# Kernel tuning notes

Hardware: AMD Instinct MI355X
Metric: run time of the kernel (lower is better)

## Reference

```python
import jax, jax.numpy as jnp
import numpy as np

N, E, G = 200000, 600000, 1024
NF_IN, EF_IN, H = 32, 16, 512
BN_EPS = 1e-5


def _bn(x, gamma, beta):
    # eval-mode BatchNorm1d with running_mean=0, running_var=1
    return x * (gamma / jnp.sqrt(1.0 + BN_EPS)) + beta


def setup_inputs() -> dict:
    key = jax.random.key(0)
    ks = jax.random.split(key, 32)
    s = 0.05
    inp = {
        'nf': jax.random.normal(ks[0], (N, NF_IN), jnp.float32),
        'ef': jax.random.normal(ks[1], (E, EF_IN), jnp.float32),
        'gf': jax.random.normal(ks[2], (G, H), jnp.float32),
        'device_params': jax.random.uniform(ks[3], (N,), jnp.float32),
        'node_y': jax.random.randint(ks[4], (N,), 0, 9),
        'batch_idx': jnp.sort(jax.random.randint(ks[5], (N,), 0, G)),
        'edge_index': jax.random.randint(ks[6], (2, E), 0, N),
        'nf_w1': jax.random.normal(ks[7], (NF_IN + 9, H), jnp.float32) * s,
        'nf_b1': jax.random.normal(ks[8], (H,), jnp.float32) * s,
        'nf_g1': jax.random.uniform(ks[9], (H,), jnp.float32, 0.5, 1.5),
        'nf_be1': jax.random.normal(ks[10], (H,), jnp.float32) * s,
        'nf_w2': jax.random.normal(ks[11], (H, H), jnp.float32) * s,
        'nf_b2': jax.random.normal(ks[12], (H,), jnp.float32) * s,
        'ef_w1': jax.random.normal(ks[13], (EF_IN, H), jnp.float32) * s,
        'ef_b1': jax.random.normal(ks[14], (H,), jnp.float32) * s,
        'ef_g1': jax.random.uniform(ks[15], (H,), jnp.float32, 0.5, 1.5),
        'ef_be1': jax.random.normal(ks[16], (H,), jnp.float32) * s,
        'ef_w2': jax.random.normal(ks[17], (H, H), jnp.float32) * s,
        'ef_b2': jax.random.normal(ks[18], (H,), jnp.float32) * s,
        'ow1': jax.random.normal(ks[19], (H, H), jnp.float32) * s,
        'ob1': jax.random.normal(ks[20], (H,), jnp.float32) * s,
        'og1': jax.random.uniform(ks[21], (H,), jnp.float32, 0.5, 1.5),
        'obe1': jax.random.normal(ks[22], (H,), jnp.float32) * s,
        'ow2': jax.random.normal(ks[23], (H, H), jnp.float32) * s,
        'ob2': jax.random.normal(ks[24], (H,), jnp.float32) * s,
        'og2': jax.random.uniform(ks[25], (H,), jnp.float32, 0.5, 1.5),
        'obe2': jax.random.normal(ks[26], (H,), jnp.float32) * s,
        'ow3': jax.random.normal(ks[27], (H, 2), jnp.float32) * s,
        'ob3': jax.random.normal(ks[28], (2,), jnp.float32) * s,
    }
    return inp


def reference(nf, ef, gf, device_params, node_y, batch_idx, edge_index,
              nf_w1, nf_b1, nf_g1, nf_be1, nf_w2, nf_b2,
              ef_w1, ef_b1, ef_g1, ef_be1, ef_w2, ef_b2,
              ow1, ob1, og1, obe1, ow2, ob2, og2, obe2, ow3, ob3):
    num_graphs = gf.shape[0]
    gelu = lambda x: jax.nn.gelu(x, approximate=False)  # torch nn.GELU default

    # DeviceParam_MLP: augment node features with scaled one-hot of node class
    nf_aug = jnp.concatenate(
        [nf, jax.nn.one_hot(node_y, 9, dtype=nf.dtype) * device_params[:, None]],
        axis=-1)  # [N, nf_in+9]
    h_n = gelu(_bn(nf_aug @ nf_w1 + nf_b1, nf_g1, nf_be1)) @ nf_w2 + nf_b2  # [N,H]
    h_e = gelu(_bn(ef @ ef_w1 + ef_b1, ef_g1, ef_be1)) @ ef_w2 + ef_b2      # [E,H]

    # two scatter_add pools into graph features
    gh = gf
    gh = gh + jax.ops.segment_sum(h_n, batch_idx, num_segments=num_graphs)
    edge_graph = batch_idx[edge_index[0]]  # graph id of each edge's source node
    gh = gh + jax.ops.segment_sum(h_e, edge_graph, num_segments=num_graphs)

    # output MLP (layer_num=3): two hidden blocks + final Linear -> 2
    x = gelu(_bn(gh @ ow1 + ob1, og1, obe1))
    x = gelu(_bn(x @ ow2 + ob2, og2, obe2))
    return x @ ow3 + ob3  # [G, 2]
```

## Files before the change

kernel.cpp:

```cpp
#include <hip/hip_runtime.h>
#include <hip/hip_bf16.h>
#include <cmath>

#define NN 200000
#define NE 600000
#define NG 1024
#define HH 512
#define ES 896

typedef short short8 __attribute__((ext_vector_type(8)));
typedef short short4v __attribute__((ext_vector_type(4)));
typedef float f32x4 __attribute__((ext_vector_type(4)));
typedef float f32x2 __attribute__((ext_vector_type(2)));
typedef float f32x16 __attribute__((ext_vector_type(16)));

__device__ __forceinline__ unsigned short f2bf(float f){
  unsigned u = __float_as_uint(f);
  u += 0x7fffu + ((u >> 16) & 1u);
  return (unsigned short)(u >> 16);
}
__device__ __forceinline__ float bf2f(unsigned short h){
  return __uint_as_float(((unsigned)h) << 16);
}

__device__ __forceinline__ short8 cvt8pk(float4 a, float4 b){
  union { short8 s; __hip_bfloat162 h[4]; } u;
  u.h[0] = __float22bfloat162_rn(make_float2(a.x, a.y));
  u.h[1] = __float22bfloat162_rn(make_float2(a.z, a.w));
  u.h[2] = __float22bfloat162_rn(make_float2(b.x, b.y));
  u.h[3] = __float22bfloat162_rn(make_float2(b.z, b.w));
  return u.s;
}

__device__ __forceinline__ float gelu_f(float x){
  float p = __builtin_fmaf(x*x, -0.10294325f, -2.3022085f);
  float e = __builtin_amdgcn_exp2f(x * p);
  return x * __builtin_amdgcn_rcpf(1.0f + e);
}

#define PKFMA3(d,a,b,c) asm("v_pk_fma_f32 %0, %1, %2, %3" : "=v"(d) : "v"(a), "v"(b), "v"(c))
#define PKFMA_IP(p,s,k) asm("v_pk_fma_f32 %0, %0, %1, %2" : "+v"(p) : "v"(s), "v"(k))
#define PKADD_IP(d,a)   asm("v_pk_add_f32 %0, %0, %1"     : "+v"(d) : "v"(a))

#define G2(y_) { \
  f32x2 s_; PKFMA3(s_, y_, y_, n1); \
  f32x2 p_; PKFMA3(p_, s_, K6, K5); \
  PKFMA_IP(p_, s_, K4); PKFMA_IP(p_, s_, K3); \
  PKFMA_IP(p_, s_, K2); PKFMA_IP(p_, s_, K1); \
  PKFMA_IP(p_, s_, K0); \
  PKADD_IP(aX, y_); PKADD_IP(aP, p_); }

#define COEFS \
  const f32x2 K0 = {c0,c0}, K1 = {c1,c1}, K2 = {c2,c2}, K3 = {c3,c3}; \
  const f32x2 K4 = {c4,c4}, K5 = {c5,c5}, K6 = {c6,c6}; \
  const f32x2 n1 = {-1.f,-1.f};

#define ISQ 0.56568542494924f
#define FXH 0.88388347648318f

__global__ __launch_bounds__(256) void kpre(
    const float* __restrict__ nfw1, const float* __restrict__ nfb1,
    const float* __restrict__ nfg1, const float* __restrict__ nfbe1,
    const float* __restrict__ efw1, const float* __restrict__ efb1,
    const float* __restrict__ efg1, const float* __restrict__ efbe1,
    const float* __restrict__ w2n, const float* __restrict__ w2e,
    const float* __restrict__ ow1, const float* __restrict__ ow2,
    unsigned short* __restrict__ w1n48T, unsigned short* __restrict__ w1eT16,
    float* __restrict__ b1n_s, float* __restrict__ b1e_s,
    const int* __restrict__ bidx, int* __restrict__ nstart,
    int* __restrict__ cnt,
    const float* __restrict__ nf, const float* __restrict__ dp,
    const int* __restrict__ ny,
    unsigned short* __restrict__ nf48,
    unsigned short* __restrict__ Bh1, unsigned short* __restrict__ Bl1,
    unsigned short* __restrict__ Bh2, unsigned short* __restrict__ Bl2,
    unsigned short* __restrict__ Bh3, unsigned short* __restrict__ Bl3){
  const float rs = 0.99999500003750f;
  int b = blockIdx.x, t = threadIdx.x;
  if (b < 2){
    int c = b*256 + t;
    float sc = efg1[c]*rs*ISQ;
#pragma unroll
    for (int k=0;k<16;++k) w1eT16[c*16+k] = f2bf(efw1[k*HH+c]*sc);
    b1e_s[c] = (efb1[c]*efg1[c]*rs + efbe1[c])*ISQ;
  } else if (b < 4){
    int c = (b-2)*256 + t;
    float sc = nfg1[c]*rs*ISQ;
#pragma unroll
    for (int k=0;k<48;++k)
      w1n48T[c*48+k] = (k < 41) ? f2bf(nfw1[k*HH+c]*sc) : (unsigned short)0;
    b1n_s[c] = (nfb1[c]*nfg1[c]*rs + nfbe1[c])*ISQ;
  } else if (b < 786){
    int i = (b-4)*256 + t;
    if (i < NN){
      int g0 = bidx[i];
      int g1 = (i+1 < NN) ? bidx[i+1] : NG;
      for (int g = g0+1; g <= g1; ++g) nstart[g] = i+1;
      if (i == 0) for (int g = 0; g <= g0; ++g) nstart[g] = 0;
    }
  } else if (b == 786){
    cnt[t] = 0; cnt[t+256] = 0; cnt[t+512] = 0; cnt[t+768] = 0;
  } else if (b < 1569){
    int r = (b-787)*256 + t;
    if (r < NN){
      const float4* ap = (const float4*)(nf + (size_t)r*32);
      unsigned short v[48];
      union { short8 s; unsigned short u[8]; } cv;
#pragma unroll
      for (int p2=0; p2<4; ++p2){
        cv.s = cvt8pk(ap[2*p2], ap[2*p2+1]);
#pragma unroll
        for (int j=0;j<8;++j) v[p2*8+j] = cv.u[j];
      }
      unsigned short db = f2bf(dp[r]);
      int cls = ny[r];
#pragma unroll
      for (int j=0;j<9;++j) v[32+j] = (cls==j) ? db : (unsigned short)0;
#pragma unroll
      for (int j=41;j<48;++j) v[j] = 0;
      unsigned short* op = nf48 + (size_t)r*48;
#pragma unroll
      for (int p2=0; p2<6; ++p2) *(short8*)(op + p2*8) = *(short8*)&v[p2*8];
    }
  } else {
    __shared__ float lds[64][65];
    int tb = b - 1569;
    int which, KK; unsigned short *Th, *Tl;
    if (tb < 128){ which = 1; KK = 1024; Th = Bh1; Tl = Bl1; }
    else if (tb < 192){ which = 2; KK = 512; Th = Bh2; Tl = Bl2; tb -= 128; }
    else { which = 3; KK = 512; Th = Bh3; Tl = Bl3; tb -= 192; }
    const int kt = tb >> 3, ct = tb & 7;
    const int k0 = kt*64, c0 = ct*64;
    const int tr = t >> 4, tc = (t & 15)*4;
#pragma unroll
    for (int i=0;i<4;++i){
      int row = tr + i*16;
      int gk = k0 + row;
      const float* src;
      if (which == 1) src = (gk < 512) ? (w2n + (size_t)gk*HH) : (w2e + (size_t)(gk-512)*HH);
      else if (which == 2) src = ow1 + (size_t)gk*HH;
      else src = ow2 + (size_t)gk*HH;
      float4 v = *(const float4*)(src + c0 + tc);
      lds[row][tc+0] = v.x; lds[row][tc+1] = v.y;
      lds[row][tc+2] = v.z; lds[row][tc+3] = v.w;
    }
    __syncthreads();
#pragma unroll
    for (int i=0;i<4;++i){
      int c = tr + i*16;
      short4v h4, l4;
#pragma unroll
      for (int j=0;j<4;++j){
        float vv = lds[tc+j][c];
        unsigned short h = f2bf(vv);
        h4[j] = (short)h;
        l4[j] = (short)f2bf(vv - bf2f(h));
      }
      size_t o = (size_t)(c0 + c)*KK + k0 + tc;
      *(short4v*)(Th + o) = h4;
      *(short4v*)(Tl + o) = l4;
    }
  }
}

__global__ __launch_bounds__(1024) void kscatter(const int* __restrict__ eidx,
    const int* __restrict__ bidx, const float* __restrict__ ef,
    int* __restrict__ eg, int* __restrict__ cnt, unsigned short* __restrict__ efs){
  __shared__ int h[NG];
  __shared__ int base[NG];
  const int b = blockIdx.x, t = threadIdx.x;
  h[t] = 0;
  __syncthreads();
  const int per = NE / 64;
  const int lo = b*per, hi = lo + per;
  for (int e = lo + t; e < hi; e += 1024){
    int g = bidx[eidx[e]];
    eg[e] = g;
    atomicAdd(&h[g], 1);
  }
  __syncthreads();
  int c = h[t];
  if (c > 0) base[t] = atomicAdd(&cnt[t], c);
  h[t] = 0;
  __syncthreads();
  for (int e = lo + t; e < hi; e += 1024){
    int g = eg[e];
    int p = base[g] + atomicAdd(&h[g], 1);
    if (p < ES){
      const float4* ap = (const float4*)(ef + (size_t)e*16);
      float4 a0 = ap[0], a1 = ap[1], a2 = ap[2], a3 = ap[3];
      unsigned short* op = efs + ((size_t)g*ES + p)*16;
      *(short8*)op       = cvt8pk(a0, a1);
      *(short8*)(op + 8) = cvt8pk(a2, a3);
    }
  }
}

__global__ __launch_bounds__(512) void kmain2(
    const unsigned short* __restrict__ efs, const int* __restrict__ cnt,
    const unsigned short* __restrict__ w1eT16, const float* __restrict__ b1e_s,
    const unsigned short* __restrict__ nf48, const int* __restrict__ nstart,
    const unsigned short* __restrict__ w1n48T, const float* __restrict__ b1n_s,
    float c0, float c1, float c2, float c3, float c4, float c5, float c6,
    unsigned short* __restrict__ Sh, unsigned short* __restrict__ Sl){
  const int t = threadIdx.x;
  const int lane = t & 63, wid = t >> 6;
  const int hi = lane >> 5, ln31 = lane & 31;
  COEFS;
  f32x2 aX = {0.f,0.f}, aP = {0.f,0.f};
  if (blockIdx.x < 2048){
    const int g = blockIdx.x >> 1;
    const int col = ((blockIdx.x & 1) << 8) + (wid << 5) + ln31;
    short8 bfr = *(const short8*)(w1eT16 + col*16 + (hi<<3));
    const float bv = b1e_s[col];
    f32x16 bias16;
#pragma unroll
    for (int i=0;i<16;++i) bias16[i] = bv;
    const int s1 = min(cnt[g], ES);
    const unsigned short* ep = efs + (size_t)g*(ES*16) + ln31*16 + (hi<<3);
    const int nfull = s1 >> 5;
    int rb = 0;
    for (int ch=0; ch<nfull; ++ch, rb += 32){
      short8 af = *(const short8*)(ep + rb*16);
      f32x16 acc = __builtin_amdgcn_mfma_f32_32x32x16_bf16(af, bfr, bias16, 0, 0, 0);
#pragma unroll
      for (int i=0;i<8;++i){
        f32x2 y = {acc[2*i], acc[2*i+1]};
        G2(y);
      }
    }
    if (rb < s1){
      int row = min(rb + ln31, s1-1);
      short8 af = *(const short8*)(efs + (size_t)g*(ES*16) + row*16 + (hi<<3));
      f32x16 acc = __builtin_amdgcn_mfma_f32_32x32x16_bf16(af, bfr, bias16, 0, 0, 0);
      const int vr = s1 - rb;
#pragma unroll
      for (int i=0;i<8;++i){
        int r0 = ((2*i)&3) + (((2*i)>>2)<<3) + (hi<<2);
        f32x2 y = { (r0 < vr) ? acc[2*i] : 0.f,
                    (r0+1 < vr) ? acc[2*i+1] : 0.f };
        G2(y);
      }
    }
    float ssum = __builtin_fmaf(FXH, aX[0]+aX[1], aP[0]+aP[1]);
    ssum += __shfl_xor(ssum, 32);
    if (lane < 32){
      size_t o = (size_t)g*1024 + 512 + col;
      unsigned short h = f2bf(ssum);
      Sh[o] = h; Sl[o] = f2bf(ssum - bf2f(h));
    }
  } else {
    const int b2 = blockIdx.x - 2048;
    const int g = b2 >> 1;
    const int col = ((b2 & 1) << 8) + (wid << 5) + ln31;
    const unsigned short* bp = w1n48T + col*48 + (hi<<3);
    short8 b0 = *(const short8*)(bp);
    short8 b1 = *(const short8*)(bp + 16);
    short8 b2f = *(const short8*)(bp + 32);
    const float bv = b1n_s[col];
    f32x16 bias16;
#pragma unroll
    for (int i=0;i<16;++i) bias16[i] = bv;
    const int s0r = nstart[g], s1 = nstart[g+1];
    const int nch = (s1 - s0r + 31) >> 5;
    for (int ch=0; ch<nch; ++ch){
      const int rb = s0r + ch*32;
      int ar = min(rb + ln31, s1-1);
      const unsigned short* apn = nf48 + (size_t)ar*48 + (hi<<3);
      short8 a0 = *(const short8*)(apn);
      short8 a1 = *(const short8*)(apn + 16);
      short8 a2 = *(const short8*)(apn + 32);
      f32x16 acc = __builtin_amdgcn_mfma_f32_32x32x16_bf16(a0, b0, bias16, 0, 0, 0);
      acc = __builtin_amdgcn_mfma_f32_32x32x16_bf16(a1, b1, acc, 0, 0, 0);
      acc = __builtin_amdgcn_mfma_f32_32x32x16_bf16(a2, b2f, acc, 0, 0, 0);
      const int vr = s1 - rb;
      if (vr >= 32){
#pragma unroll
        for (int i=0;i<8;++i){
          f32x2 y = {acc[2*i], acc[2*i+1]};
          G2(y);
        }
      } else {
#pragma unroll
        for (int i=0;i<8;++i){
          int r0 = ((2*i)&3) + (((2*i)>>2)<<3) + (hi<<2);
          f32x2 y = { (r0 < vr) ? acc[2*i] : 0.f,
                      (r0+1 < vr) ? acc[2*i+1] : 0.f };
          G2(y);
        }
      }
    }
    float ssum = __builtin_fmaf(FXH, aX[0]+aX[1], aP[0]+aP[1]);
    ssum += __shfl_xor(ssum, 32);
    if (lane < 32){
      size_t o = (size_t)g*1024 + col;
      unsigned short h = f2bf(ssum);
      Sh[o] = h; Sl[o] = f2bf(ssum - bf2f(h));
    }
  }
}

__global__ __launch_bounds__(256) void kg(
    const unsigned short* __restrict__ Ah, const unsigned short* __restrict__ Al,
    int K, int nkc,
    const unsigned short* __restrict__ Bh, const unsigned short* __restrict__ Bl,
    const float* __restrict__ gf, const int* __restrict__ nstart, const int* __restrict__ cnt,
    const float* __restrict__ b2n, const float* __restrict__ b2e,
    const float* __restrict__ bias, const float* __restrict__ gam, const float* __restrict__ bet,
    unsigned short* __restrict__ Oh, unsigned short* __restrict__ Ol,
    float* __restrict__ outf){
  const int t = threadIdx.x, lane = t & 63, w = t >> 6;
  const int q = lane >> 4, m = lane & 15;
  const int flat = blockIdx.y*32 + blockIdx.x;
  const int swz = (flat & 7)*64 + (flat >> 3);
  const int c0 = (swz & 31)*16, r0 = (swz >> 5)*64 + w*16;
  f32x4 acc = {0.f,0.f,0.f,0.f};
  const unsigned short* ahp = Ah + (size_t)(r0 + m)*K + (q<<3);
  const unsigned short* alp = Al + (size_t)(r0 + m)*K + (q<<3);
  const unsigned short* bhp = Bh + (size_t)(c0 + m)*K + (q<<3);
  const unsigned short* blp = Bl + (size_t)(c0 + m)*K + (q<<3);
#pragma unroll 2
  for (int kc = 0; kc < nkc; ++kc){
    const int ko = kc*32;
    short8 ah = *(const short8*)(ahp + ko);
    short8 al = *(const short8*)(alp + ko);
    short8 bh = *(const short8*)(bhp + ko);
    short8 bl = *(const short8*)(blp + ko);
    acc = __builtin_amdgcn_mfma_f32_16x16x32_bf16(ah, bh, acc, 0, 0, 0);
    acc = __builtin_amdgcn_mfma_f32_16x16x32_bf16(ah, bl, acc, 0, 0, 0);
    acc = __builtin_amdgcn_mfma_f32_16x16x32_bf16(al, bh, acc, 0, 0, 0);
  }
  const float rs = 0.99999500003750f;
  const int c = c0 + m;
  if (gf){
    const float bnv = b2n[c], bev = b2e[c];
#pragma unroll
    for (int i=0;i<4;++i){
      int r = r0 + q*4 + i;
      float cn = (float)(nstart[r+1] - nstart[r]);
      float ce = (float)min(cnt[r], ES);
      float v = acc[i] + gf[(size_t)r*HH + c] + cn*bnv + ce*bev;
      unsigned short h = f2bf(v);
      Oh[(size_t)r*HH + c] = h;
      Ol[(size_t)r*HH + c] = f2bf(v - bf2f(h));
    }
  } else {
    const float sc = gam[c]*rs, bi = bias[c], be = bet[c];
#pragma unroll
    for (int i=0;i<4;++i){
      int r = r0 + q*4 + i;
      float v = gelu_f((acc[i] + bi)*sc + be);
      if (outf) outf[(size_t)r*HH + c] = v;
      else {
        unsigned short h = f2bf(v);
        Oh[(size_t)r*HH + c] = h;
        Ol[(size_t)r*HH + c] = f2bf(v - bf2f(h));
      }
    }
  }
}

__global__ __launch_bounds__(256) void kfinal(const float* __restrict__ x2, const float* __restrict__ w3,
    const float* __restrict__ b3, float* __restrict__ out){
  const int lane = threadIdx.x & 63, wv = threadIdx.x >> 6;
  const int r = blockIdx.x*4 + wv;
  float a0 = 0.f, a1 = 0.f;
#pragma unroll
  for (int tt=0; tt<8; ++tt){
    int k = lane + tt*64;
    float x = x2[(size_t)r*HH + k];
    a0 = __builtin_fmaf(x, w3[2*k], a0);
    a1 = __builtin_fmaf(x, w3[2*k+1], a1);
  }
#pragma unroll
  for (int d=1; d<64; d<<=1){ a0 += __shfl_xor(a0, d); a1 += __shfl_xor(a1, d); }
  if (lane == 0){ out[r*2] = a0 + b3[0]; out[r*2+1] = a1 + b3[1]; }
}

extern "C" void kernel_launch(void* const* d_in, const int* in_sizes, int n_in,
                              void* d_out, int out_size, void* d_ws, size_t ws_size,
                              hipStream_t stream) {
  const float* nf    = (const float*)d_in[0];
  const float* ef    = (const float*)d_in[1];
  const float* gf    = (const float*)d_in[2];
  const float* dp    = (const float*)d_in[3];
  const int*   ny    = (const int*)d_in[4];
  const int*   bidx  = (const int*)d_in[5];
  const int*   eidx  = (const int*)d_in[6];
  const float* nfw1  = (const float*)d_in[7];
  const float* nfb1  = (const float*)d_in[8];
  const float* nfg1  = (const float*)d_in[9];
  const float* nfbe1 = (const float*)d_in[10];
  const float* w2n   = (const float*)d_in[11];
  const float* b2n   = (const float*)d_in[12];
  const float* efw1  = (const float*)d_in[13];
  const float* efb1  = (const float*)d_in[14];
  const float* efg1  = (const float*)d_in[15];
  const float* efbe1 = (const float*)d_in[16];
  const float* w2e   = (const float*)d_in[17];
  const float* b2e   = (const float*)d_in[18];
  const float* ow1   = (const float*)d_in[19];
  const float* ob1   = (const float*)d_in[20];
  const float* og1   = (const float*)d_in[21];
  const float* obe1  = (const float*)d_in[22];
  const float* ow2   = (const float*)d_in[23];
  const float* ob2   = (const float*)d_in[24];
  const float* og2   = (const float*)d_in[25];
  const float* obe2  = (const float*)d_in[26];
  const float* ow3   = (const float*)d_in[27];
  const float* ob3   = (const float*)d_in[28];

  static float MC[7];
  static bool inited = false;
  if (!inited){
    const double PI = 3.14159265358979323846;
    double th[7], fj[7];
    for (int j=0;j<7;++j){
      th[j] = PI*((double)j + 0.5)/7.0;
      double u = 3.125*(cos(th[j]) + 1.0);
      double v = sqrt(u);
      fj[j] = 0.5*v*erf(v*0.70710678118654752);
    }
    double c[7];
    for (int k=0;k<7;++k){
      double sm = 0.0;
      for (int j=0;j<7;++j) sm += fj[j]*cos((double)k*th[j]);
      c[k] = 2.0*sm/7.0;
    }
    c[0] *= 0.5;
    const double T[7][7] = {
      { 1, 0,  0,  0,   0,  0,  0},
      { 0, 1,  0,  0,   0,  0,  0},
      {-1, 0,  2,  0,   0,  0,  0},
      { 0,-3,  0,  4,   0,  0,  0},
      { 1, 0, -8,  0,   8,  0,  0},
      { 0, 5,  0,-20,   0, 16,  0},
      {-1, 0, 18,  0, -48,  0, 32}};
    double m[7] = {0,0,0,0,0,0,0};
    for (int k=0;k<7;++k)
      for (int i=0;i<7;++i) m[i] += c[k]*T[k][i];
    double p1 = m[0]-m[1]+m[2]-m[3]+m[4]-m[5]+m[6];
    m[0] -= p1;
    for (int i=0;i<7;++i) MC[i] = (float)m[i];
    inited = true;
  }

  unsigned char* p = (unsigned char*)d_ws;
  unsigned short* Sh = (unsigned short*)p;   p += (size_t)NG*1024*2;
  unsigned short* Sl = (unsigned short*)p;   p += (size_t)NG*1024*2;
  unsigned short* efs = (unsigned short*)p;  p += (size_t)NG*ES*16*2;
  unsigned short* nf48 = (unsigned short*)p; p += (size_t)NN*48*2;
  unsigned short* Bh1 = (unsigned short*)p;  p += (size_t)HH*1024*2;
  unsigned short* Bl1 = (unsigned short*)p;  p += (size_t)HH*1024*2;
  unsigned short* Bh2 = (unsigned short*)p;  p += (size_t)HH*512*2;
  unsigned short* Bl2 = (unsigned short*)p;  p += (size_t)HH*512*2;
  unsigned short* Bh3 = (unsigned short*)p;  p += (size_t)HH*512*2;
  unsigned short* Bl3 = (unsigned short*)p;  p += (size_t)HH*512*2;
  unsigned short* w1n48T = (unsigned short*)p; p += 512*48*2;
  unsigned short* w1eT16 = (unsigned short*)p; p += 512*16*2;
  float* b1n_s  = (float*)p;                 p += 512*4;
  float* b1e_s  = (float*)p;                 p += 512*4;
  int* nstart   = (int*)p;                   p += 1032*4;
  int* cnt      = (int*)p;                   p += NG*4;
  int* eg = (int*)Sh;
  unsigned short* ghh = (unsigned short*)nf48;
  unsigned short* ghl = ghh + (size_t)NG*HH;
  unsigned short* xgh = ghl + (size_t)NG*HH;
  unsigned short* xgl = xgh + (size_t)NG*HH;
  float* x2f = (float*)(xgl + (size_t)NG*HH);

  kpre<<<1825, 256, 0, stream>>>(nfw1, nfb1, nfg1, nfbe1, efw1, efb1, efg1, efbe1,
                                 w2n, w2e, ow1, ow2,
                                 w1n48T, w1eT16, b1n_s, b1e_s, bidx, nstart, cnt,
                                 nf, dp, ny, nf48,
                                 Bh1, Bl1, Bh2, Bl2, Bh3, Bl3);
  kscatter<<<64, 1024, 0, stream>>>(eidx, bidx, ef, eg, cnt, efs);
  kmain2<<<4096, 512, 0, stream>>>(efs, cnt, w1eT16, b1e_s,
                                   nf48, nstart, w1n48T, b1n_s,
                                   MC[0], MC[1], MC[2], MC[3], MC[4], MC[5], MC[6],
                                   Sh, Sl);
  kg<<<dim3(32,16), 256, 0, stream>>>(Sh, Sl, 1024, 32, Bh1, Bl1,
                                      gf, nstart, cnt, b2n, b2e,
                                      nullptr, nullptr, nullptr, ghh, ghl, nullptr);
  kg<<<dim3(32,16), 256, 0, stream>>>(ghh, ghl, 512, 16, Bh2, Bl2,
                                      nullptr, nullptr, nullptr, nullptr, nullptr,
                                      ob1, og1, obe1, xgh, xgl, nullptr);
  kg<<<dim3(32,16), 256, 0, stream>>>(xgh, xgl, 512, 16, Bh3, Bl3,
                                      nullptr, nullptr, nullptr, nullptr, nullptr,
                                      ob2, og2, obe2, nullptr, nullptr, x2f);
  kfinal<<<NG/4, 256, 0, stream>>>(x2f, ow3, ob3, (float*)d_out);
}
```

Measured before the change: 372.9 us.

## Fuse final linear layer into last GEMM epilogue and prefetch edge tiles

Removes the separate final kernel. The last GEMM epilogue now multiplies each GELU output by the two output weights, reduces across the 16 columns with shuffles, and atomically adds into the output, which kpre pre-fills with the bias. It also software-prefetches the next 32-row edge tile in the edge MLP loop and pads the edge buffer so the overrun read stays in bounds. This saves a kernel launch and the fp32 intermediate round trip, at the cost of float atomics that make the summation order nondeterministic.

```diff
diff --git a/kernel.cpp b/kernel.cpp
--- a/kernel.cpp
+++ b/kernel.cpp
@@ -65,6 +65,7 @@
     const float* __restrict__ efg1, const float* __restrict__ efbe1,
     const float* __restrict__ w2n, const float* __restrict__ w2e,
     const float* __restrict__ ow1, const float* __restrict__ ow2,
+    const float* __restrict__ ob3, float* __restrict__ outd,
     unsigned short* __restrict__ w1n48T, unsigned short* __restrict__ w1eT16,
     float* __restrict__ b1n_s, float* __restrict__ b1e_s,
     const int* __restrict__ bidx, int* __restrict__ nstart,
@@ -100,6 +101,8 @@
     }
   } else if (b == 786){
     cnt[t] = 0; cnt[t+256] = 0; cnt[t+512] = 0; cnt[t+768] = 0;
+    float bb0 = ob3[0], bb1 = ob3[1];
+    for (int i = t; i < 2048; i += 256) outd[i] = (i & 1) ? bb1 : bb0;
   } else if (b < 1569){
     int r = (b-787)*256 + t;
     if (r < NN){
@@ -218,28 +221,30 @@
     for (int i=0;i<16;++i) bias16[i] = bv;
     const int s1 = min(cnt[g], ES);
     const unsigned short* ep = efs + (size_t)g*(ES*16) + ln31*16 + (hi<<3);
-    const int nfull = s1 >> 5;
-    int rb = 0;
-    for (int ch=0; ch<nfull; ++ch, rb += 32){
-      short8 af = *(const short8*)(ep + rb*16);
-      f32x16 acc = __builtin_amdgcn_mfma_f32_32x32x16_bf16(af, bfr, bias16, 0, 0, 0);
-#pragma unroll
-      for (int i=0;i<8;++i){
-        f32x2 y = {acc[2*i], acc[2*i+1]};
-        G2(y);
-      }
-    }
-    if (rb < s1){
-      int row = min(rb + ln31, s1-1);
-      short8 af = *(const short8*)(efs + (size_t)g*(ES*16) + row*16 + (hi<<3));
-      f32x16 acc = __builtin_amdgcn_mfma_f32_32x32x16_bf16(af, bfr, bias16, 0, 0, 0);
-      const int vr = s1 - rb;
-#pragma unroll
-      for (int i=0;i<8;++i){
-        int r0 = ((2*i)&3) + (((2*i)>>2)<<3) + (hi<<2);
-        f32x2 y = { (r0 < vr) ? acc[2*i] : 0.f,
-                    (r0+1 < vr) ? acc[2*i+1] : 0.f };
-        G2(y);
+    if (s1 > 0){
+      const int nfull = s1 >> 5;
+      int rb = 0;
+      short8 afc = *(const short8*)(ep);
+      for (int ch=0; ch<nfull; ++ch, rb += 32){
+        short8 afn = *(const short8*)(ep + (size_t)(rb+32)*16);
+        f32x16 acc = __builtin_amdgcn_mfma_f32_32x32x16_bf16(afc, bfr, bias16, 0, 0, 0);
+#pragma unroll
+        for (int i=0;i<8;++i){
+          f32x2 y = {acc[2*i], acc[2*i+1]};
+          G2(y);
+        }
+        afc = afn;
+      }
+      if (rb < s1){
+        f32x16 acc = __builtin_amdgcn_mfma_f32_32x32x16_bf16(afc, bfr, bias16, 0, 0, 0);
+        const int vr = s1 - rb;
+#pragma unroll
+        for (int i=0;i<8;++i){
+          int r0 = ((2*i)&3) + (((2*i)>>2)<<3) + (hi<<2);
+          f32x2 y = { (r0 < vr) ? acc[2*i] : 0.f,
+                      (r0+1 < vr) ? acc[2*i+1] : 0.f };
+          G2(y);
+        }
       }
     }
     float ssum = __builtin_fmaf(FXH, aX[0]+aX[1], aP[0]+aP[1]);
@@ -308,7 +313,7 @@
     const float* __restrict__ b2n, const float* __restrict__ b2e,
     const float* __restrict__ bias, const float* __restrict__ gam, const float* __restrict__ bet,
     unsigned short* __restrict__ Oh, unsigned short* __restrict__ Ol,
-    float* __restrict__ outf){
+    const float* __restrict__ w3f, float* __restrict__ outp){
   const int t = threadIdx.x, lane = t & 63, w = t >> 6;
   const int q = lane >> 4, m = lane & 15;
   const int flat = blockIdx.y*32 + blockIdx.x;
@@ -344,37 +349,34 @@
       Oh[(size_t)r*HH + c] = h;
       Ol[(size_t)r*HH + c] = f2bf(v - bf2f(h));
     }
-  } else {
+  } else if (w3f){
     const float sc = gam[c]*rs, bi = bias[c], be = bet[c];
+    const float w0 = w3f[2*c], w1 = w3f[2*c+1];
 #pragma unroll
     for (int i=0;i<4;++i){
       int r = r0 + q*4 + i;
       float v = gelu_f((acc[i] + bi)*sc + be);
-      if (outf) outf[(size_t)r*HH + c] = v;
-      else {
-        unsigned short h = f2bf(v);
-        Oh[(size_t)r*HH + c] = h;
-        Ol[(size_t)r*HH + c] = f2bf(v - bf2f(h));
-      }
-    }
-  }
-}
-
-__global__ __launch_bounds__(256) void kfinal(const float* __restrict__ x2, const float* __restrict__ w3,
-    const float* __restrict__ b3, float* __restrict__ out){
-  const int lane = threadIdx.x & 63, wv = threadIdx.x >> 6;
-  const int r = blockIdx.x*4 + wv;
-  float a0 = 0.f, a1 = 0.f;
-#pragma unroll
-  for (int tt=0; tt<8; ++tt){
-    int k = lane + tt*64;
-    float x = x2[(size_t)r*HH + k];
-    a0 = __builtin_fmaf(x, w3[2*k], a0);
-    a1 = __builtin_fmaf(x, w3[2*k+1], a1);
-  }
-#pragma unroll
-  for (int d=1; d<64; d<<=1){ a0 += __shfl_xor(a0, d); a1 += __shfl_xor(a1, d); }
-  if (lane == 0){ out[r*2] = a0 + b3[0]; out[r*2+1] = a1 + b3[1]; }
+      float p0 = v*w0, p1 = v*w1;
+      p0 += __shfl_xor(p0, 1); p0 += __shfl_xor(p0, 2);
+      p0 += __shfl_xor(p0, 4); p0 += __shfl_xor(p0, 8);
+      p1 += __shfl_xor(p1, 1); p1 += __shfl_xor(p1, 2);
+      p1 += __shfl_xor(p1, 4); p1 += __shfl_xor(p1, 8);
+      if (m == 0){
+        atomicAdd(&outp[r*2],   p0);
+        atomicAdd(&outp[r*2+1], p1);
+      }
+    }
+  } else {
+    const float sc = gam[c]*rs, bi = bias[c], be = bet[c];
+#pragma unroll
+    for (int i=0;i<4;++i){
+      int r = r0 + q*4 + i;
+      float v = gelu_f((acc[i] + bi)*sc + be);
+      unsigned short h = f2bf(v);
+      Oh[(size_t)r*HH + c] = h;
+      Ol[(size_t)r*HH + c] = f2bf(v - bf2f(h));
+    }
+  }
 }
 
 extern "C" void kernel_launch(void* const* d_in, const int* in_sizes, int n_in,
@@ -448,7 +450,7 @@
   unsigned char* p = (unsigned char*)d_ws;
   unsigned short* Sh = (unsigned short*)p;   p += (size_t)NG*1024*2;
   unsigned short* Sl = (unsigned short*)p;   p += (size_t)NG*1024*2;
-  unsigned short* efs = (unsigned short*)p;  p += (size_t)NG*ES*16*2;
+  unsigned short* efs = (unsigned short*)p;  p += ((size_t)NG*ES + 64)*16*2;
   unsigned short* nf48 = (unsigned short*)p; p += (size_t)NN*48*2;
   unsigned short* Bh1 = (unsigned short*)p;  p += (size_t)HH*1024*2;
   unsigned short* Bl1 = (unsigned short*)p;  p += (size_t)HH*1024*2;
@@ -467,10 +469,9 @@
   unsigned short* ghl = ghh + (size_t)NG*HH;
   unsigned short* xgh = ghl + (size_t)NG*HH;
   unsigned short* xgl = xgh + (size_t)NG*HH;
-  float* x2f = (float*)(xgl + (size_t)NG*HH);
 
   kpre<<<1825, 256, 0, stream>>>(nfw1, nfb1, nfg1, nfbe1, efw1, efb1, efg1, efbe1,
-                                 w2n, w2e, ow1, ow2,
+                                 w2n, w2e, ow1, ow2, ob3, (float*)d_out,
                                  w1n48T, w1eT16, b1n_s, b1e_s, bidx, nstart, cnt,
                                  nf, dp, ny, nf48,
                                  Bh1, Bl1, Bh2, Bl2, Bh3, Bl3);
@@ -481,12 +482,14 @@
                                    Sh, Sl);
   kg<<<dim3(32,16), 256, 0, stream>>>(Sh, Sl, 1024, 32, Bh1, Bl1,
                                       gf, nstart, cnt, b2n, b2e,
-                                      nullptr, nullptr, nullptr, ghh, ghl, nullptr);
+                                      nullptr, nullptr, nullptr, ghh, ghl,
+                                      nullptr, nullptr);
   kg<<<dim3(32,16), 256, 0, stream>>>(ghh, ghl, 512, 16, Bh2, Bl2,
                                       nullptr, nullptr, nullptr, nullptr, nullptr,
-                                      ob1, og1, obe1, xgh, xgl, nullptr);
+                                      ob1, og1, obe1, xgh, xgl,
+                                      nullptr, nullptr);
   kg<<<dim3(32,16), 256, 0, stream>>>(xgh, xgl, 512, 16, Bh3, Bl3,
                                       nullptr, nullptr, nullptr, nullptr, nullptr,
-                                      ob2, og2, obe2, nullptr, nullptr, x2f);
-  kfinal<<<NG/4, 256, 0, stream>>>(x2f, ow3, ob3, (float*)d_out);
-}
+                                      ob2, og2, obe2, nullptr, nullptr,
+                                      ow3, (float*)d_out);
+}
```

New measurement: 374.7 us. No clear change (+0.5%).
